# Kernel optimization log

Hardware: AMD Instinct MI355X
Metric: run time of the kernel (lower is better)

Reference implementation:

```python
import jax, jax.numpy as jnp
import numpy as np


def setup_inputs() -> dict:
    key = jax.random.key(0)
    k1, k2, k3 = jax.random.split(key, 3)
    B, L, I = 128, 512, 1024
    doc_rep = jax.random.normal(k1, (B, L, I), dtype=jnp.float32)
    # torch.nn.Linear(input_size, label_size): weight (L, I), bias (L,)
    W = jax.random.normal(k2, (L, I), dtype=jnp.float32) * (1.0 / np.sqrt(I))
    b = jax.random.normal(k3, (L,), dtype=jnp.float32) * 0.01
    return {"doc_rep": doc_rep, "W": W, "b": b}


def reference(doc_rep, W, b):
    # Original: full Linear -> (B, L, L), then take diagonal over last two dims.
    # Diagonal of (doc_rep @ W.T + b) is exactly the per-label dot product:
    # out[b, l] = doc_rep[b, l, :] . W[l, :] + b[l]
    logits = jnp.einsum('bli,li->bl', doc_rep, W) + b
    return jax.nn.sigmoid(logits)
```

## Files before the change

kernel.cpp:

```cpp
#include <hip/hip_runtime.h>
#include <hip/hip_bf16.h>


#define B_DIM 128
#define L_DIM 512
#define I_DIM 1024
#define WPB 8

typedef float vfloat4 __attribute__((ext_vector_type(4)));

__global__ __launch_bounds__(256) void labelwise_mlc_kernel(
    const float* __restrict__ doc,
    const float* __restrict__ W,
    const float* __restrict__ bias,
    float* __restrict__ out)
{
    const int wave = (blockIdx.x * 256 + threadIdx.x) >> 6;
    const int lane = threadIdx.x & 63;
    const int l  = wave & (L_DIM - 1);
    const int b0 = (wave >> 9) * WPB;

    const vfloat4* __restrict__ wp = (const vfloat4*)(W + (size_t)l * I_DIM);
    vfloat4 w[4];
#pragma unroll
    for (int k = 0; k < 4; ++k) w[k] = wp[lane + 64 * k];
    const float bl = bias[l];

#pragma unroll 2
    for (int j = 0; j < WPB; ++j) {
        const int b = b0 + j;
        const vfloat4* __restrict__ dp =
            (const vfloat4*)(doc + ((size_t)b * L_DIM + l) * I_DIM);
        float acc = 0.0f;
#pragma unroll
        for (int k = 0; k < 4; ++k) {
            const vfloat4 d = __builtin_nontemporal_load(dp + lane + 64 * k);
            acc = fmaf(d.x, w[k].x, acc);
            acc = fmaf(d.y, w[k].y, acc);
            acc = fmaf(d.z, w[k].z, acc);
            acc = fmaf(d.w, w[k].w, acc);
        }
#pragma unroll
        for (int off = 32; off > 0; off >>= 1)
            acc += __shfl_down(acc, off, 64);
        if (lane == 0) {
            const float v = acc + bl;
            out[(size_t)b * L_DIM + l] = 1.0f / (1.0f + __expf(-v));
        }
    }
}

extern "C" void kernel_launch(void* const* d_in, const int* in_sizes, int n_in,
                              void* d_out, int out_size, void* d_ws, size_t ws_size,
                              hipStream_t stream) {
    const float* doc  = (const float*)d_in[0];
    const float* W    = (const float*)d_in[1];
    const float* bias = (const float*)d_in[2];
    float* out = (float*)d_out;

    const int blocks = (L_DIM * (B_DIM / WPB)) / 4;
    labelwise_mlc_kernel<<<blocks, 256, 0, stream>>>(doc, W, bias, out);
}
```

Before: 333.0 us.

## Double-buffer doc rows into LDS via async global_load_lds

Replaces direct nontemporal vector loads of doc rows with asynchronous global-to-LDS loads, double-buffered per wave, with manual waitcnt to overlap the next row's fetch with the current dot product. Each wave now processes 16 batch rows instead of 8, halving the grid. This is meant to keep more memory traffic in flight while hiding load latency, but it adds LDS round-trips, hand-encoded waitcnt fragility, and fewer resident waves.

```diff
diff --git a/kernel.cpp b/kernel.cpp
--- a/kernel.cpp
+++ b/kernel.cpp
@@ -5,9 +5,21 @@
 #define B_DIM 128
 #define L_DIM 512
 #define I_DIM 1024
-#define WPB 8
+#define WPB 16
+#define WAVES_PER_BLOCK 4
 
 typedef float vfloat4 __attribute__((ext_vector_type(4)));
+
+__device__ __forceinline__ void async_row_load(const float* g, float* l,
+                                               int lane) {
+#pragma unroll
+    for (int k = 0; k < 4; ++k) {
+        __builtin_amdgcn_global_load_lds(
+            (const __attribute__((address_space(1))) void*)(g + k * 256 + lane * 4),
+            (__attribute__((address_space(3))) void*)(l + k * 256),
+            16, 0, 0);
+    }
+}
 
 __global__ __launch_bounds__(256) void labelwise_mlc_kernel(
     const float* __restrict__ doc,
@@ -15,10 +27,22 @@
     const float* __restrict__ bias,
     float* __restrict__ out)
 {
-    const int wave = (blockIdx.x * 256 + threadIdx.x) >> 6;
+    __shared__ float smem[WAVES_PER_BLOCK][2][I_DIM];
+
+    const int wid  = threadIdx.x >> 6;
     const int lane = threadIdx.x & 63;
-    const int l  = wave & (L_DIM - 1);
-    const int b0 = (wave >> 9) * WPB;
+    const int gw   = blockIdx.x * WAVES_PER_BLOCK + wid;
+    const int l    = gw & (L_DIM - 1);
+    const int b0   = (gw >> 9) * WPB;
+
+    const size_t rstride = (size_t)L_DIM * I_DIM;
+    const float* rowbase = doc + ((size_t)b0 * L_DIM + l) * I_DIM;
+
+    float* buf0 = &smem[wid][0][0];
+    float* buf1 = &smem[wid][1][0];
+
+    async_row_load(rowbase, buf0, lane);
+    async_row_load(rowbase + rstride, buf1, lane);
 
     const vfloat4* __restrict__ wp = (const vfloat4*)(W + (size_t)l * I_DIM);
     vfloat4 w[4];
@@ -26,26 +50,32 @@
     for (int k = 0; k < 4; ++k) w[k] = wp[lane + 64 * k];
     const float bl = bias[l];
 
-#pragma unroll 2
     for (int j = 0; j < WPB; ++j) {
-        const int b = b0 + j;
-        const vfloat4* __restrict__ dp =
-            (const vfloat4*)(doc + ((size_t)b * L_DIM + l) * I_DIM);
+        if (j < WPB - 1) __builtin_amdgcn_s_waitcnt(0xF74);
+        else             __builtin_amdgcn_s_waitcnt(0xF70);
+
+        const float* lb = (j & 1) ? buf1 : buf0;
         float acc = 0.0f;
 #pragma unroll
         for (int k = 0; k < 4; ++k) {
-            const vfloat4 d = __builtin_nontemporal_load(dp + lane + 64 * k);
+            const vfloat4 d = ((const vfloat4*)lb)[lane + 64 * k];
             acc = fmaf(d.x, w[k].x, acc);
             acc = fmaf(d.y, w[k].y, acc);
             acc = fmaf(d.z, w[k].z, acc);
             acc = fmaf(d.w, w[k].w, acc);
         }
+
+        __builtin_amdgcn_s_waitcnt(0xC07F);
+        if (j + 2 < WPB)
+            async_row_load(rowbase + (size_t)(j + 2) * rstride,
+                           (j & 1) ? buf1 : buf0, lane);
+
 #pragma unroll
         for (int off = 32; off > 0; off >>= 1)
             acc += __shfl_down(acc, off, 64);
         if (lane == 0) {
             const float v = acc + bl;
-            out[(size_t)b * L_DIM + l] = 1.0f / (1.0f + __expf(-v));
+            out[(size_t)(b0 + j) * L_DIM + l] = 1.0f / (1.0f + __expf(-v));
         }
     }
 }
@@ -58,6 +88,6 @@
     const float* bias = (const float*)d_in[2];
     float* out = (float*)d_out;
 
-    const int blocks = (L_DIM * (B_DIM / WPB)) / 4;
+    const int blocks = (L_DIM * (B_DIM / WPB)) / WAVES_PER_BLOCK;
     labelwise_mlc_kernel<<<blocks, 256, 0, stream>>>(doc, W, bias, out);
 }
```

Measured after the change: 357.2 us. 7.3% more time.
